# Kernel optimization log

Hardware: AMD Instinct MI355X
Metric: run time of the kernel (lower is better)

Reference implementation:

```python
import jax, jax.numpy as jnp
import numpy as np

B, S, D = 4, 2048, 1024
H, DK, DV = 16, 64, 64


def setup_inputs() -> dict:
    key = jax.random.key(0)
    ks = jax.random.split(key, 9)
    std = 1.0 / np.sqrt(D)
    inp = {
        "x": jax.random.normal(ks[0], (B, S, D), jnp.float32),
        "c": jax.random.normal(ks[1], (B, S, D), jnp.float32),
        "Wq_x": jax.random.normal(ks[2], (D, H * DK), jnp.float32) * std,
        "Wk_x": jax.random.normal(ks[3], (D, H * DK), jnp.float32) * std,
        "Wv_x": jax.random.normal(ks[4], (D, H * DV), jnp.float32) * std,
        "Wq_c": jax.random.normal(ks[5], (D, H * DK), jnp.float32) * std,
        "Wk_c": jax.random.normal(ks[6], (D, H * DK), jnp.float32) * std,
        "Wv_c": jax.random.normal(ks[7], (D, H * DV), jnp.float32) * std,
        "W_proj": jax.random.normal(ks[8], (2 * H * DV, D), jnp.float32) * (1.0 / np.sqrt(2 * H * DV)),
        "b_proj": jnp.zeros((D,), jnp.float32),
    }
    return inp


def _heads(t, hd):
    # [B,S,H*hd] -> [B,H,S,hd]
    b, s, _ = t.shape
    return t.reshape(b, s, H, hd).transpose(0, 2, 1, 3)


def reference(x, c, Wq_x, Wk_x, Wv_x, Wq_c, Wk_c, Wv_c, W_proj, b_proj):
    q = jnp.concatenate([_heads(x @ Wq_x, DK), _heads(c @ Wq_c, DK)], axis=-1)  # [B,H,S,2DK]
    k = jnp.concatenate([_heads(x @ Wk_x, DK), _heads(c @ Wk_c, DK)], axis=-1)
    v = jnp.concatenate([_heads(x @ Wv_x, DV), _heads(c @ Wv_c, DV)], axis=-1)  # [B,H,S,2DV]
    # NOTE: original scales by sqrt(k_dim), not sqrt(2*k_dim) (faithful)
    scores = jnp.einsum("bhqd,bhkd->bhqk", q, k) / np.float32(np.sqrt(DK))
    attn = jax.nn.softmax(scores, axis=-1)
    out = jnp.einsum("bhqk,bhkd->bhqd", attn, v)  # [B,H,S,2DV]
    out = out.transpose(0, 2, 1, 3).reshape(x.shape[0], x.shape[1], -1)  # [B,S,H*2DV]
    return out @ W_proj + b_proj
```

## Files before the change

### kernel.cpp

```cpp
#include <hip/hip_runtime.h>
#include <hip/hip_bf16.h>
#include <stdint.h>

#define BB 4
#define SS 2048
#define DD 1024
#define HH 16
#define DHH 128

typedef __bf16 bf16x8 __attribute__((ext_vector_type(8)));
typedef __bf16 bf16x4 __attribute__((ext_vector_type(4)));
typedef float  f32x4  __attribute__((ext_vector_type(4)));

#define SL2E 0.180336880111186f

#if __has_builtin(__builtin_amdgcn_exp2f)
#define EXP2(x) __builtin_amdgcn_exp2f(x)
#else
#define EXP2(x) exp2f(x)
#endif

#define GLOAD_LDS16(gp, lp) \
  __builtin_amdgcn_global_load_lds((const __attribute__((address_space(1))) unsigned int*)(gp), \
                                   (__attribute__((address_space(3))) unsigned int*)(lp), 16, 0, 0)

#define SBAR() do { asm volatile("" ::: "memory"); \
                    __builtin_amdgcn_s_barrier();  \
                    asm volatile("" ::: "memory"); } while (0)

__global__ void cast2_kernel(const float* __restrict__ x, const float* __restrict__ c,
                             __bf16* __restrict__ out, int n) {
    int i = (blockIdx.x * blockDim.x + threadIdx.x) * 4;
    const float* src = (i < n) ? (x + i) : (c + (i - n));
    f32x4 v = *(const f32x4*)src;
    bf16x4 o;
    o[0] = (__bf16)v[0]; o[1] = (__bf16)v[1]; o[2] = (__bf16)v[2]; o[3] = (__bf16)v[3];
    *(bf16x4*)(out + i) = o;
}

__global__ void transpose_cast_kernel(const float* __restrict__ in, __bf16* __restrict__ out,
                                      int K, int N) {
    __shared__ float tile[32][33];
    int n0 = blockIdx.x * 32, k0 = blockIdx.y * 32;
    int tx = threadIdx.x, ty = threadIdx.y;
    #pragma unroll
    for (int i = 0; i < 32; i += 8)
        tile[ty + i][tx] = in[(size_t)(k0 + ty + i) * N + n0 + tx];
    __syncthreads();
    #pragma unroll
    for (int i = 0; i < 32; i += 8)
        out[(size_t)(n0 + ty + i) * K + k0 + tx] = (__bf16)tile[tx][ty + i];
}

__global__ void transpose6_kernel(const float* s0, const float* s1, const float* s2,
                                  const float* s3, const float* s4, const float* s5,
                                  __bf16* __restrict__ dst) {
    const float* srcs[6] = {s0, s1, s2, s3, s4, s5};
    const float* __restrict__ in = srcs[blockIdx.z];
    __bf16* __restrict__ out = dst + (size_t)blockIdx.z * 1024 * 1024;
    __shared__ float tile[32][33];
    int n0 = blockIdx.x * 32, k0 = blockIdx.y * 32;
    int tx = threadIdx.x, ty = threadIdx.y;
    #pragma unroll
    for (int i = 0; i < 32; i += 8)
        tile[ty + i][tx] = in[(size_t)(k0 + ty + i) * 1024 + n0 + tx];
    __syncthreads();
    #pragma unroll
    for (int i = 0; i < 32; i += 8)
        out[(size_t)(n0 + ty + i) * 1024 + k0 + tx] = (__bf16)tile[tx][ty + i];
}

template <int EPI>
__global__ __launch_bounds__(512, 2)
void gemm256_kernel(const __bf16* __restrict__ A0, const __bf16* __restrict__ A1,
                    const __bf16* __restrict__ B0, const __bf16* __restrict__ B1,
                    int K, void* __restrict__ outp, const float* __restrict__ bias) {
    const int z = blockIdx.z;
    const __bf16* __restrict__ A  = z ? A1 : A0;
    const __bf16* __restrict__ Bt = z ? B1 : B0;
    const int qkv_off = z * 64;

    __shared__ __align__(16) char smem[131072];

    const int tid = threadIdx.x;
    const int wave = tid >> 6, lane = tid & 63;
    const int l15 = lane & 15, quad = lane >> 4;
    const int wr = wave >> 2, wc = wave & 3;

    const int gx = gridDim.x;
    const int nwg = gx * gridDim.y;
    const int hwl = blockIdx.y * gx + blockIdx.x;
    const int lg  = (hwl & 7) * (nwg >> 3) + (hwl >> 3);
    const int m0 = (lg % gx) * 256, n0 = (lg / gx) * 256;

    const int rA = tid >> 2;
    const int cs = (tid & 3) ^ ((tid >> 4) & 3);
    const __bf16* aS0 = A  + (size_t)(m0 + rA) * K + cs * 8;
    const __bf16* aS1 = aS0 + (size_t)128 * K;
    const __bf16* bS0 = Bt + (size_t)(n0 + rA) * K + cs * 8;
    const __bf16* bS1 = bS0 + (size_t)128 * K;
    const int ldsA = wave * 1024;
    const int ldsB = 16384 + wave * 1024;

    const int swz = ((quad ^ (l15 >> 2)) & 3) * 16;
    const int ra = (wr * 128 + l15) * 64 + swz;
    const int rb = 16384 + (wc * 64 + l15) * 64 + swz;

    f32x4 acc[8][4] = {};
    const int NT = K >> 5;

    #define STAGE_A(tt) do { const int bo_ = ((tt) & 3) * 32768; \
        GLOAD_LDS16(aS0 + (size_t)(tt) * 32, smem + bo_ + ldsA); \
        GLOAD_LDS16(aS1 + (size_t)(tt) * 32, smem + bo_ + ldsA + 8192); } while (0)
    #define STAGE_B(tt) do { const int bo_ = ((tt) & 3) * 32768; \
        GLOAD_LDS16(bS0 + (size_t)(tt) * 32, smem + bo_ + ldsB); \
        GLOAD_LDS16(bS1 + (size_t)(tt) * 32, smem + bo_ + ldsB + 8192); } while (0)

    STAGE_A(0); STAGE_B(0);
    STAGE_A(1); STAGE_B(1);
    STAGE_A(2); STAGE_B(2);
    asm volatile("s_waitcnt vmcnt(8)" ::: "memory");
    SBAR();

    for (int t = 0; t < NT; ++t) {
        const int co = (t & 3) * 32768;
        bf16x8 af[4], bfr[4];
        #pragma unroll
        for (int i = 0; i < 4; ++i) af[i]  = *(const bf16x8*)(smem + co + ra + i * 1024);
        #pragma unroll
        for (int i = 0; i < 4; ++i) bfr[i] = *(const bf16x8*)(smem + co + rb + i * 1024);
        if (t + 3 < NT) STAGE_A(t + 3);
        SBAR();
        __builtin_amdgcn_s_setprio(1);
        #pragma unroll
        for (int mi = 0; mi < 4; ++mi)
            #pragma unroll
            for (int ni = 0; ni < 4; ++ni)
                acc[mi][ni] = __builtin_amdgcn_mfma_f32_16x16x32_bf16(af[mi], bfr[ni], acc[mi][ni], 0, 0, 0);
        __builtin_amdgcn_s_setprio(0);
        SBAR();
        #pragma unroll
        for (int i = 0; i < 4; ++i) af[i] = *(const bf16x8*)(smem + co + ra + (4 + i) * 1024);
        if (t + 3 < NT) STAGE_B(t + 3);
        SBAR();
        __builtin_amdgcn_s_setprio(1);
        #pragma unroll
        for (int mi = 0; mi < 4; ++mi)
            #pragma unroll
            for (int ni = 0; ni < 4; ++ni)
                acc[4 + mi][ni] = __builtin_amdgcn_mfma_f32_16x16x32_bf16(af[mi], bfr[ni], acc[4 + mi][ni], 0, 0, 0);
        __builtin_amdgcn_s_setprio(0);
        if (t < NT - 3)       asm volatile("s_waitcnt vmcnt(8)" ::: "memory");
        else if (t == NT - 3) asm volatile("s_waitcnt vmcnt(4)" ::: "memory");
        else if (t == NT - 2) asm volatile("s_waitcnt vmcnt(0)" ::: "memory");
        SBAR();
    }
    #undef STAGE_A
    #undef STAGE_B

    const size_t nQKV = (size_t)BB * HH * SS * DHH;
    #pragma unroll
    for (int mi = 0; mi < 8; ++mi) {
        #pragma unroll
        for (int ni = 0; ni < 4; ++ni) {
            #pragma unroll
            for (int rr = 0; rr < 4; ++rr) {
                int m = m0 + wr * 128 + mi * 16 + quad * 4 + rr;
                int n = n0 + wc * 64 + ni * 16 + l15;
                if (EPI == 1) {
                    float* o = (float*)outp;
                    o[(size_t)m * 1024 + n] = acc[mi][ni][rr] + bias[n];
                } else if (EPI == 2) {
                    int h = m >> 6, dl = m & 63;
                    int b = n >> 11, s = n & (SS - 1);
                    __bf16* vt = (__bf16*)outp;
                    vt[(((size_t)b * HH + h) * DHH + dl + qkv_off) * SS + s] = (__bf16)acc[mi][ni][rr];
                } else {
                    int b = m >> 11, s = m & (SS - 1);
                    int n1 = n & 1023;
                    int h = n1 >> 6, d = (n1 & 63) + qkv_off;
                    if (n < 1024) {
                        __bf16* q = (__bf16*)outp;
                        q[(((size_t)b * HH + h) * SS + s) * DHH + d] = (__bf16)(acc[mi][ni][rr] * SL2E);
                    } else {
                        int dsw = (((d >> 3) ^ (s & 15)) << 3) | (d & 7);
                        __bf16* kq = (__bf16*)outp + nQKV;
                        kq[(((size_t)b * HH + h) * SS + s) * DHH + dsw] = (__bf16)acc[mi][ni][rr];
                    }
                }
            }
        }
    }
}

#define LDS_BUFSZ 32768
#define LDS_VT    16384
#define LDS_PS    65536
__global__ __launch_bounds__(256, 2)
void attn_kernel(const __bf16* __restrict__ Q, const __bf16* __restrict__ Kg,
                 const __bf16* __restrict__ Vg, __bf16* __restrict__ O, int bh0) {
    __shared__ __align__(16) char smem[73728];

    const int t = threadIdx.x;
    const int wave = t >> 6, lane = t & 63;
    const int l15 = lane & 15, quad = lane >> 4;

    const int lin = blockIdx.x;
    const int slot = lin >> 3, xcd = lin & 7;
    const int mt = slot & 15;
    const int bh = bh0 + ((slot >> 4) << 3) + xcd;

    const int b = bh >> 4, h = bh & 15;
    const size_t base  = (size_t)bh * SS * DHH;
    const size_t vbase = (size_t)bh * DHH * SS;

    int kaddr[4];
    #pragma unroll
    for (int kst = 0; kst < 4; ++kst)
        kaddr[kst] = l15 * 256 + (((4 * kst + quad) ^ l15) & 15) * 16;
    int vaddr[2];
    #pragma unroll
    for (int hf = 0; hf < 2; ++hf)
        vaddr[hf] = LDS_VT + l15 * 128 + (((4 * hf + quad) ^ (l15 & 7)) & 7) * 16;
    int pw[2];
    #pragma unroll
    for (int nl = 0; nl < 2; ++nl)
        pw[nl] = LDS_PS + (wave * 32 + quad * 4) * 64 +
                 (((2 * nl + (l15 >> 3)) ^ quad) & 3) * 16 + (l15 & 7) * 2;
    const int par = LDS_PS + (wave * 32 + l15) * 64 + ((quad ^ (l15 >> 2)) & 3) * 16;

    const __bf16* kstage = Kg + base + (size_t)wave * 2048 + lane * 8;
    const __bf16* vstage = Vg + vbase + (size_t)(wave * 32 + (lane >> 3)) * SS
                           + ((lane & 7) ^ ((lane >> 3) & 7)) * 8;

    #define STAGE_KV(kt_, bo_) do { \
        _Pragma("unroll") \
        for (int i_ = 0; i_ < 4; ++i_) \
            GLOAD_LDS16(kstage + (size_t)(kt_) * 8192 + i_ * 512, \
                        smem + (bo_) + wave * 4096 + i_ * 1024); \
        _Pragma("unroll") \
        for (int i_ = 0; i_ < 4; ++i_) \
            GLOAD_LDS16(vstage + (kt_) * 64 + (size_t)i_ * 8 * SS, \
                        smem + (bo_) + LDS_VT + wave * 4096 + i_ * 1024); \
    } while (0)

    bf16x8 qf[2][4];
    #pragma unroll
    for (int ms = 0; ms < 2; ++ms) {
        int row = mt * 128 + wave * 32 + ms * 16 + l15;
        #pragma unroll
        for (int kst = 0; kst < 4; ++kst)
            qf[ms][kst] = *(const bf16x8*)(Q + base + (size_t)row * DHH + kst * 32 + quad * 8);
    }

    f32x4 oacc[2][8] = {};
    float li_[2][4] = {};

    STAGE_KV(0, 0);
    __syncthreads();

    for (int kt = 0; kt < SS / 64; ++kt) {
        const int co = (kt & 1) * LDS_BUFSZ;
        if (kt + 1 < SS / 64) STAGE_KV(kt + 1, co ^ LDS_BUFSZ);

        #pragma unroll
        for (int hf = 0; hf < 2; ++hf) {
            f32x4 sx[2][2] = {};
            __builtin_amdgcn_s_setprio(1);
            #pragma unroll
            for (int kst = 0; kst < 4; ++kst) {
                bf16x8 kf0 = *(const bf16x8*)(smem + co + kaddr[kst] + 8192 * hf);
                bf16x8 kf1 = *(const bf16x8*)(smem + co + kaddr[kst] + 8192 * hf + 4096);
                sx[0][0] = __builtin_amdgcn_mfma_f32_16x16x32_bf16(qf[0][kst], kf0, sx[0][0], 0, 0, 0);
                sx[1][0] = __builtin_amdgcn_mfma_f32_16x16x32_bf16(qf[1][kst], kf0, sx[1][0], 0, 0, 0);
                sx[0][1] = __builtin_amdgcn_mfma_f32_16x16x32_bf16(qf[0][kst], kf1, sx[0][1], 0, 0, 0);
                sx[1][1] = __builtin_amdgcn_mfma_f32_16x16x32_bf16(qf[1][kst], kf1, sx[1][1], 0, 0, 0);
            }
            __builtin_amdgcn_s_setprio(0);
            #pragma unroll
            for (int ms = 0; ms < 2; ++ms)
                #pragma unroll
                for (int nl = 0; nl < 2; ++nl)
                    #pragma unroll
                    for (int rr = 0; rr < 4; ++rr) {
                        float p = EXP2(sx[ms][nl][rr]);
                        li_[ms][rr] += p;
                        sx[ms][nl][rr] = p;
                    }

            #pragma unroll
            for (int ms = 0; ms < 2; ++ms)
                #pragma unroll
                for (int nl = 0; nl < 2; ++nl)
                    #pragma unroll
                    for (int rr = 0; rr < 4; ++rr)
                        *(__bf16*)(smem + pw[nl] + 1024 * ms + 64 * rr)
                            = (__bf16)sx[ms][nl][rr];

            bf16x8 pa0 = *(const bf16x8*)(smem + par);
            bf16x8 pa1 = *(const bf16x8*)(smem + par + 1024);
            __builtin_amdgcn_s_setprio(1);
            #pragma unroll
            for (int ds = 0; ds < 8; ++ds) {
                bf16x8 vf = *(const bf16x8*)(smem + co + vaddr[hf] + 2048 * ds);
                oacc[0][ds] = __builtin_amdgcn_mfma_f32_16x16x32_bf16(pa0, vf, oacc[0][ds], 0, 0, 0);
                oacc[1][ds] = __builtin_amdgcn_mfma_f32_16x16x32_bf16(pa1, vf, oacc[1][ds], 0, 0, 0);
            }
            __builtin_amdgcn_s_setprio(0);
        }
        __syncthreads();
    }
    #undef STAGE_KV

    #pragma unroll
    for (int ms = 0; ms < 2; ++ms)
        #pragma unroll
        for (int rr = 0; rr < 4; ++rr) {
            float v = li_[ms][rr];
            v += __shfl_xor(v, 1);
            v += __shfl_xor(v, 2);
            v += __shfl_xor(v, 4);
            v += __shfl_xor(v, 8);
            li_[ms][rr] = 1.f / v;
        }

    #pragma unroll
    for (int ms = 0; ms < 2; ++ms)
        #pragma unroll
        for (int rr = 0; rr < 4; ++rr) {
            int s = mt * 128 + wave * 32 + ms * 16 + quad * 4 + rr;
            size_t ob = ((size_t)b * SS + s) * (HH * DHH) + (size_t)h * DHH;
            #pragma unroll
            for (int ds = 0; ds < 8; ++ds)
                O[ob + ds * 16 + l15] = (__bf16)(oacc[ms][ds][rr] * li_[ms][rr]);
        }
}

extern "C" void kernel_launch(void* const* d_in, const int* in_sizes, int n_in,
                              void* d_out, int out_size, void* d_ws, size_t ws_size,
                              hipStream_t stream) {
    const float* x      = (const float*)d_in[0];
    const float* c      = (const float*)d_in[1];
    const float* Wq_x   = (const float*)d_in[2];
    const float* Wk_x   = (const float*)d_in[3];
    const float* Wv_x   = (const float*)d_in[4];
    const float* Wq_c   = (const float*)d_in[5];
    const float* Wk_c   = (const float*)d_in[6];
    const float* Wv_c   = (const float*)d_in[7];
    const float* W_proj = (const float*)d_in[8];
    const float* b_proj = (const float*)d_in[9];

    const size_t nXC  = (size_t)BB * SS * DD;
    const size_t nW   = (size_t)DD * DD;
    const size_t nWP  = (size_t)(2 * HH * 64) * DD;
    const size_t nQKV = (size_t)BB * HH * SS * DHH;

    __bf16* ws  = (__bf16*)d_ws;
    __bf16* xb  = ws;
    __bf16* cb  = xb + nXC;
    __bf16* wt0 = cb + nXC;
    __bf16* wt2 = wt0 + 2 * nW;
    __bf16* wt3 = wt0 + 3 * nW;
    __bf16* wt5 = wt0 + 5 * nW;
    __bf16* wtp = wt0 + 6 * nW;
    __bf16* Qb  = wtp + nWP;
    __bf16* Kb  = Qb + nQKV;
    __bf16* Vb  = Kb + nQKV;
    __bf16* Ob  = xb;

    cast2_kernel<<<(int)(2 * nXC / 1024), 256, 0, stream>>>(x, c, xb, (int)nXC);

    transpose6_kernel<<<dim3(32, 32, 6), dim3(32, 8), 0, stream>>>(
        Wq_x, Wk_x, Wv_x, Wq_c, Wk_c, Wv_c, wt0);
    transpose_cast_kernel<<<dim3(32, 64), dim3(32, 8), 0, stream>>>(W_proj, wtp, 2048, 1024);

    gemm256_kernel<4><<<dim3(32, 8, 2), 512, 0, stream>>>(xb, cb, wt0, wt3, 1024, Qb, nullptr);
    gemm256_kernel<2><<<dim3(4, 32, 2), 512, 0, stream>>>(wt2, wt5, xb, cb, 1024, Vb, nullptr);

    attn_kernel<<<dim3(512), 256, 0, stream>>>(Qb, Kb, Vb, Ob, 0);
    attn_kernel<<<dim3(512), 256, 0, stream>>>(Qb, Kb, Vb, Ob, 32);

    gemm256_kernel<1><<<dim3(32, 4, 1), 512, 0, stream>>>(Ob, nullptr, wtp, nullptr, 2048, d_out, b_proj);
}
```

Measured before the change: 487.6 us.

## Double-buffer GEMM fragments, merge attention launches, add 256x128 projection GEMM

The main GEMM loop now prefetches the next k-step's A/B register fragments while the MFMAs for the current step run, and it drops one barrier per iteration so LDS reads overlap compute. A dedicated projection GEMM with 256x128 tiles replaces the 256x256 EPI=1 path, which doubles the block count for the output projection (128 to 256 blocks) so more CUs are occupied. The two half-size attention launches are merged into a single 1024-block launch to cut launch overhead and the tail between them. The cost is higher register pressure from the duplicated fragment buffers, plus a risk of LDS races now that fewer barriers guard the buffers.

Result: faster. 447.5 us (-8.2%).

```diff
diff --git a/kernel.cpp b/kernel.cpp
--- a/kernel.cpp
+++ b/kernel.cpp
@@ -27,6 +27,8 @@
 #define SBAR() do { asm volatile("" ::: "memory"); \
                     __builtin_amdgcn_s_barrier();  \
                     asm volatile("" ::: "memory"); } while (0)
+
+#define MFMA_BF16(a, b, c) __builtin_amdgcn_mfma_f32_16x16x32_bf16((a), (b), (c), 0, 0, 0)
 
 __global__ void cast2_kernel(const float* __restrict__ x, const float* __restrict__ c,
                              __bf16* __restrict__ out, int n) {
@@ -107,6 +109,7 @@
     const int rb = 16384 + (wc * 64 + l15) * 64 + swz;
 
     f32x4 acc[8][4] = {};
+    bf16x8 afc[2][4], bfc[2][4], afB[4];
     const int NT = K >> 5;
 
     #define STAGE_A(tt) do { const int bo_ = ((tt) & 3) * 32768; \
@@ -121,39 +124,48 @@
     STAGE_A(2); STAGE_B(2);
     asm volatile("s_waitcnt vmcnt(8)" ::: "memory");
     SBAR();
-
-    for (int t = 0; t < NT; ++t) {
-        const int co = (t & 3) * 32768;
-        bf16x8 af[4], bfr[4];
-        #pragma unroll
-        for (int i = 0; i < 4; ++i) af[i]  = *(const bf16x8*)(smem + co + ra + i * 1024);
-        #pragma unroll
-        for (int i = 0; i < 4; ++i) bfr[i] = *(const bf16x8*)(smem + co + rb + i * 1024);
-        if (t + 3 < NT) STAGE_A(t + 3);
-        SBAR();
-        __builtin_amdgcn_s_setprio(1);
-        #pragma unroll
-        for (int mi = 0; mi < 4; ++mi)
-            #pragma unroll
-            for (int ni = 0; ni < 4; ++ni)
-                acc[mi][ni] = __builtin_amdgcn_mfma_f32_16x16x32_bf16(af[mi], bfr[ni], acc[mi][ni], 0, 0, 0);
-        __builtin_amdgcn_s_setprio(0);
-        SBAR();
-        #pragma unroll
-        for (int i = 0; i < 4; ++i) af[i] = *(const bf16x8*)(smem + co + ra + (4 + i) * 1024);
-        if (t + 3 < NT) STAGE_B(t + 3);
-        SBAR();
-        __builtin_amdgcn_s_setprio(1);
-        #pragma unroll
-        for (int mi = 0; mi < 4; ++mi)
-            #pragma unroll
-            for (int ni = 0; ni < 4; ++ni)
-                acc[4 + mi][ni] = __builtin_amdgcn_mfma_f32_16x16x32_bf16(af[mi], bfr[ni], acc[4 + mi][ni], 0, 0, 0);
-        __builtin_amdgcn_s_setprio(0);
-        if (t < NT - 3)       asm volatile("s_waitcnt vmcnt(8)" ::: "memory");
-        else if (t == NT - 3) asm volatile("s_waitcnt vmcnt(4)" ::: "memory");
-        else if (t == NT - 2) asm volatile("s_waitcnt vmcnt(0)" ::: "memory");
-        SBAR();
+    #pragma unroll
+    for (int i = 0; i < 4; ++i) afc[0][i] = *(const bf16x8*)(smem + ra + i * 1024);
+    #pragma unroll
+    for (int i = 0; i < 4; ++i) bfc[0][i] = *(const bf16x8*)(smem + rb + i * 1024);
+
+    for (int tp = 0; tp < NT / 2; ++tp) {
+        #pragma unroll
+        for (int u = 0; u < 2; ++u) {
+            const int t = 2 * tp + u;
+            const int co = (t & 3) * 32768;
+            const int cn = ((t + 1) & 3) * 32768;
+            #pragma unroll
+            for (int i = 0; i < 4; ++i)
+                afB[i] = *(const bf16x8*)(smem + co + ra + (4 + i) * 1024);
+            if (t + 3 < NT) STAGE_A(t + 3);
+            SBAR();
+            __builtin_amdgcn_s_setprio(1);
+            #pragma unroll
+            for (int mi = 0; mi < 4; ++mi)
+                #pragma unroll
+                for (int ni = 0; ni < 4; ++ni)
+                    acc[mi][ni] = MFMA_BF16(afc[u][mi], bfc[u][ni], acc[mi][ni]);
+            __builtin_amdgcn_s_setprio(0);
+            if (t + 3 < NT) STAGE_B(t + 3);
+            if (t < NT - 3)       asm volatile("s_waitcnt vmcnt(8)" ::: "memory");
+            else if (t == NT - 3) asm volatile("s_waitcnt vmcnt(4)" ::: "memory");
+            else if (t == NT - 2) asm volatile("s_waitcnt vmcnt(0)" ::: "memory");
+            SBAR();
+            #pragma unroll
+            for (int i = 0; i < 4; ++i)
+                afc[u ^ 1][i] = *(const bf16x8*)(smem + cn + ra + i * 1024);
+            #pragma unroll
+            for (int i = 0; i < 4; ++i)
+                bfc[u ^ 1][i] = *(const bf16x8*)(smem + cn + rb + i * 1024);
+            __builtin_amdgcn_s_setprio(1);
+            #pragma unroll
+            for (int mi = 0; mi < 4; ++mi)
+                #pragma unroll
+                for (int ni = 0; ni < 4; ++ni)
+                    acc[4 + mi][ni] = MFMA_BF16(afB[mi], bfc[u][ni], acc[4 + mi][ni]);
+            __builtin_amdgcn_s_setprio(0);
+        }
     }
     #undef STAGE_A
     #undef STAGE_B
@@ -167,10 +179,7 @@
             for (int rr = 0; rr < 4; ++rr) {
                 int m = m0 + wr * 128 + mi * 16 + quad * 4 + rr;
                 int n = n0 + wc * 64 + ni * 16 + l15;
-                if (EPI == 1) {
-                    float* o = (float*)outp;
-                    o[(size_t)m * 1024 + n] = acc[mi][ni][rr] + bias[n];
-                } else if (EPI == 2) {
+                if (EPI == 2) {
                     int h = m >> 6, dl = m & 63;
                     int b = n >> 11, s = n & (SS - 1);
                     __bf16* vt = (__bf16*)outp;
@@ -193,12 +202,96 @@
     }
 }
 
+__global__ __launch_bounds__(512, 2)
+void gemm_proj_kernel(const __bf16* __restrict__ A, const __bf16* __restrict__ Bt,
+                      int K, float* __restrict__ outp, const float* __restrict__ bias) {
+    __shared__ __align__(16) char smem[98304];
+
+    const int tid = threadIdx.x;
+    const int wave = tid >> 6, lane = tid & 63;
+    const int l15 = lane & 15, quad = lane >> 4;
+    const int wr = wave >> 1, wc = wave & 1;
+
+    const int gx = gridDim.x;
+    const int nwg = gx * gridDim.y;
+    const int hwl = blockIdx.y * gx + blockIdx.x;
+    const int lg  = (hwl & 7) * (nwg >> 3) + (hwl >> 3);
+    const int m0 = (lg % gx) * 256, n0 = (lg / gx) * 128;
+
+    const int rA = tid >> 2;
+    const int cs = (tid & 3) ^ ((tid >> 4) & 3);
+    const __bf16* aS0 = A  + (size_t)(m0 + rA) * K + cs * 8;
+    const __bf16* aS1 = aS0 + (size_t)128 * K;
+    const __bf16* bS0 = Bt + (size_t)(n0 + rA) * K + cs * 8;
+    const int ldsA = wave * 1024;
+    const int ldsB = 16384 + wave * 1024;
+
+    const int swz = ((quad ^ (l15 >> 2)) & 3) * 16;
+    const int ra = (wr * 64 + l15) * 64 + swz;
+    const int rb = 16384 + (wc * 64 + l15) * 64 + swz;
+
+    f32x4 acc[4][4] = {};
+    bf16x8 afc[2][4], bfc[2][4];
+    const int NT = K >> 5;
+
+    #define STAGE_P(tt) do { const int bo_ = ((tt) & 3) * 24576; \
+        GLOAD_LDS16(aS0 + (size_t)(tt) * 32, smem + bo_ + ldsA); \
+        GLOAD_LDS16(aS1 + (size_t)(tt) * 32, smem + bo_ + ldsA + 8192); \
+        GLOAD_LDS16(bS0 + (size_t)(tt) * 32, smem + bo_ + ldsB); } while (0)
+
+    STAGE_P(0); STAGE_P(1); STAGE_P(2);
+    asm volatile("s_waitcnt vmcnt(6)" ::: "memory");
+    SBAR();
+    #pragma unroll
+    for (int i = 0; i < 4; ++i) afc[0][i] = *(const bf16x8*)(smem + ra + i * 1024);
+    #pragma unroll
+    for (int i = 0; i < 4; ++i) bfc[0][i] = *(const bf16x8*)(smem + rb + i * 1024);
+
+    for (int tp = 0; tp < NT / 2; ++tp) {
+        #pragma unroll
+        for (int u = 0; u < 2; ++u) {
+            const int t = 2 * tp + u;
+            const int cn = ((t + 1) & 3) * 24576;
+            if (t + 3 < NT) STAGE_P(t + 3);
+            if (t < NT - 3)       asm volatile("s_waitcnt vmcnt(6)" ::: "memory");
+            else if (t == NT - 3) asm volatile("s_waitcnt vmcnt(3)" ::: "memory");
+            else if (t == NT - 2) asm volatile("s_waitcnt vmcnt(0)" ::: "memory");
+            SBAR();
+            #pragma unroll
+            for (int i = 0; i < 4; ++i)
+                afc[u ^ 1][i] = *(const bf16x8*)(smem + cn + ra + i * 1024);
+            #pragma unroll
+            for (int i = 0; i < 4; ++i)
+                bfc[u ^ 1][i] = *(const bf16x8*)(smem + cn + rb + i * 1024);
+            __builtin_amdgcn_s_setprio(1);
+            #pragma unroll
+            for (int mi = 0; mi < 4; ++mi)
+                #pragma unroll
+                for (int ni = 0; ni < 4; ++ni)
+                    acc[mi][ni] = MFMA_BF16(afc[u][mi], bfc[u][ni], acc[mi][ni]);
+            __builtin_amdgcn_s_setprio(0);
+        }
+    }
+    #undef STAGE_P
+
+    #pragma unroll
+    for (int mi = 0; mi < 4; ++mi)
+        #pragma unroll
+        for (int ni = 0; ni < 4; ++ni)
+            #pragma unroll
+            for (int rr = 0; rr < 4; ++rr) {
+                int m = m0 + wr * 64 + mi * 16 + quad * 4 + rr;
+                int n = n0 + wc * 64 + ni * 16 + l15;
+                outp[(size_t)m * 1024 + n] = acc[mi][ni][rr] + bias[n];
+            }
+}
+
 #define LDS_BUFSZ 32768
 #define LDS_VT    16384
 #define LDS_PS    65536
 __global__ __launch_bounds__(256, 2)
 void attn_kernel(const __bf16* __restrict__ Q, const __bf16* __restrict__ Kg,
-                 const __bf16* __restrict__ Vg, __bf16* __restrict__ O, int bh0) {
+                 const __bf16* __restrict__ Vg, __bf16* __restrict__ O) {
     __shared__ __align__(16) char smem[73728];
 
     const int t = threadIdx.x;
@@ -206,9 +299,8 @@
     const int l15 = lane & 15, quad = lane >> 4;
 
     const int lin = blockIdx.x;
-    const int slot = lin >> 3, xcd = lin & 7;
-    const int mt = slot & 15;
-    const int bh = bh0 + ((slot >> 4) << 3) + xcd;
+    const int mt = (lin >> 3) & 15;
+    const int bh = ((lin >> 7) << 3) + (lin & 7);
 
     const int b = bh >> 4, h = bh & 15;
     const size_t base  = (size_t)bh * SS * DHH;
@@ -271,10 +363,10 @@
             for (int kst = 0; kst < 4; ++kst) {
                 bf16x8 kf0 = *(const bf16x8*)(smem + co + kaddr[kst] + 8192 * hf);
                 bf16x8 kf1 = *(const bf16x8*)(smem + co + kaddr[kst] + 8192 * hf + 4096);
-                sx[0][0] = __builtin_amdgcn_mfma_f32_16x16x32_bf16(qf[0][kst], kf0, sx[0][0], 0, 0, 0);
-                sx[1][0] = __builtin_amdgcn_mfma_f32_16x16x32_bf16(qf[1][kst], kf0, sx[1][0], 0, 0, 0);
-                sx[0][1] = __builtin_amdgcn_mfma_f32_16x16x32_bf16(qf[0][kst], kf1, sx[0][1], 0, 0, 0);
-                sx[1][1] = __builtin_amdgcn_mfma_f32_16x16x32_bf16(qf[1][kst], kf1, sx[1][1], 0, 0, 0);
+                sx[0][0] = MFMA_BF16(qf[0][kst], kf0, sx[0][0]);
+                sx[1][0] = MFMA_BF16(qf[1][kst], kf0, sx[1][0]);
+                sx[0][1] = MFMA_BF16(qf[0][kst], kf1, sx[0][1]);
+                sx[1][1] = MFMA_BF16(qf[1][kst], kf1, sx[1][1]);
             }
             __builtin_amdgcn_s_setprio(0);
             #pragma unroll
@@ -303,8 +395,8 @@
             #pragma unroll
             for (int ds = 0; ds < 8; ++ds) {
                 bf16x8 vf = *(const bf16x8*)(smem + co + vaddr[hf] + 2048 * ds);
-                oacc[0][ds] = __builtin_amdgcn_mfma_f32_16x16x32_bf16(pa0, vf, oacc[0][ds], 0, 0, 0);
-                oacc[1][ds] = __builtin_amdgcn_mfma_f32_16x16x32_bf16(pa1, vf, oacc[1][ds], 0, 0, 0);
+                oacc[0][ds] = MFMA_BF16(pa0, vf, oacc[0][ds]);
+                oacc[1][ds] = MFMA_BF16(pa1, vf, oacc[1][ds]);
             }
             __builtin_amdgcn_s_setprio(0);
         }
@@ -377,8 +469,7 @@
     gemm256_kernel<4><<<dim3(32, 8, 2), 512, 0, stream>>>(xb, cb, wt0, wt3, 1024, Qb, nullptr);
     gemm256_kernel<2><<<dim3(4, 32, 2), 512, 0, stream>>>(wt2, wt5, xb, cb, 1024, Vb, nullptr);
 
-    attn_kernel<<<dim3(512), 256, 0, stream>>>(Qb, Kb, Vb, Ob, 0);
-    attn_kernel<<<dim3(512), 256, 0, stream>>>(Qb, Kb, Vb, Ob, 32);
-
-    gemm256_kernel<1><<<dim3(32, 4, 1), 512, 0, stream>>>(Ob, nullptr, wtp, nullptr, 2048, d_out, b_proj);
-}
+    attn_kernel<<<dim3(1024), 256, 0, stream>>>(Qb, Kb, Vb, Ob);
+
+    gemm_proj_kernel<<<dim3(32, 8), 512, 0, stream>>>(Ob, wtp, 2048, (float*)d_out, b_proj);
+}
```
